# Kernel optimization log

Hardware: AMD Instinct MI355X
Metric: run time of the kernel (lower is better)

## Reference

```python
import jax, jax.numpy as jnp
import numpy as np

N = 50000
E = 800000
IN_DIM = 128
HID = 256
NCLASS = 40
ORDER = 3
LOCAL_NOISE = 0.5


def setup_inputs() -> dict:
    key = jax.random.key(0)
    ks = jax.random.split(key, 8)
    feats = jax.random.normal(ks[0], (N, IN_DIM), dtype=jnp.float32)
    edge_row = jax.random.randint(ks[1], (E,), 0, N, dtype=jnp.int32)
    edge_col = jax.random.randint(ks[2], (E,), 0, N, dtype=jnp.int32)
    edge_vals = jax.random.uniform(ks[3], (E,), dtype=jnp.float32) / 16.0  # ~row-normalized adjacency
    W1 = jax.random.normal(ks[4], (IN_DIM, HID), dtype=jnp.float32) * (1.0 / np.sqrt(IN_DIM))
    b1 = jnp.zeros((HID,), dtype=jnp.float32)
    W2 = jax.random.normal(ks[5], (HID, NCLASS), dtype=jnp.float32) * (1.0 / np.sqrt(HID))
    b2 = jnp.zeros((NCLASS,), dtype=jnp.float32)
    return {"feats": feats, "edge_row": edge_row, "edge_col": edge_col,
            "edge_vals": edge_vals, "W1": W1, "b1": b1, "W2": W2, "b2": b2}


def _spmm(edge_row, edge_col, edge_vals, x):
    # y[r] = sum_e vals[e] * x[col[e]] for edges with row[e]==r
    msgs = edge_vals[:, None] * x[edge_col]  # [E, D]
    return jax.ops.segment_sum(msgs, edge_row, num_segments=N)


def reference(feats, edge_row, edge_col, edge_vals, W1, b1, W2, b2):
    # eval path: drop_node scales by (1 - drop_rate)
    x = feats * (1.0 - LOCAL_NOISE)
    # GRANDConv_NX: K-hop propagation with running-sum average
    y = x
    h = x
    for _ in range(ORDER):
        h = _spmm(edge_row, edge_col, edge_vals, h)
        y = y + h
    feat = y / (ORDER + 1.0)
    # MLP (use_bn=False, dropout inactive at eval)
    h1 = jax.nn.relu(feat @ W1 + b1)
    logits = h1 @ W2 + b2
    # MLP.forward applies log_softmax, outer forward applies it again
    out = jax.nn.log_softmax(jax.nn.log_softmax(logits, axis=-1), axis=-1)
    return out
```

## Files before the change

kernel.cpp:

```cpp
#include <hip/hip_runtime.h>
#include <math.h>

#define N_NODES 50000
#define N_EDGES 800000
#define IN_DIM 128
#define HID 256
#define NCLASS 40

#define SCAN_NBLK 49

#define HBLK 256
#define EPB  3125
#define PK   12500

typedef __attribute__((ext_vector_type(8))) short short8;
typedef __attribute__((ext_vector_type(4))) float floatx4;

__device__ inline unsigned bf16pair(float a, float b) {
    unsigned ua = __float_as_uint(a), ub = __float_as_uint(b);
    ua = (ua + 0x7fffu + ((ua >> 16) & 1u)) >> 16;
    ub = (ub + 0x7fffu + ((ub >> 16) & 1u)) >> 16;
    return ua | (ub << 16);
}
__device__ inline unsigned bf16bits(float a) {
    unsigned ua = __float_as_uint(a);
    return (ua + 0x7fffu + ((ua >> 16) & 1u)) >> 16;
}
__device__ inline float bf_lo(unsigned u) { return __uint_as_float(u << 16); }
__device__ inline float bf_hi(unsigned u) { return __uint_as_float(u & 0xffff0000u); }

__global__ void prep_kernel(const float4* __restrict__ f4,
                            uint2* __restrict__ fb16,
                            const float* __restrict__ W1,
                            uint4* __restrict__ W1frag) {
    int i = blockIdx.x * blockDim.x + threadIdx.x;
    float4 v = f4[i];
    fb16[i] = make_uint2(bf16pair(v.x, v.y), bf16pair(v.z, v.w));
    if (i < 4096) {
        int f = i;
        int h = f >> 11, rem = f & 2047;
        int t = rem >> 8, s = (rem >> 6) & 3, l = rem & 63;
        int q = l >> 4, n16 = l & 15;
        int n = h * 128 + t * 16 + n16;
        int kb = s * 32 + q * 8;
        unsigned p[4];
        #pragma unroll
        for (int jj = 0; jj < 4; ++jj) {
            float a = W1[(size_t)(kb + 2 * jj) * HID + n];
            float b = W1[(size_t)(kb + 2 * jj + 1) * HID + n];
            p[jj] = bf16pair(a, b);
        }
        W1frag[f] = make_uint4(p[0], p[1], p[2], p[3]);
    }
}

__global__ __launch_bounds__(1024) void hist_kernel(const int* __restrict__ rows,
                                                    unsigned* __restrict__ hist) {
    __shared__ unsigned h[PK];
    int t = threadIdx.x;
    for (int i = t; i < PK / 4; i += 1024)
        ((uint4*)h)[i] = make_uint4(0u, 0u, 0u, 0u);
    __syncthreads();
    int e0 = blockIdx.x * EPB;
    for (int i = t; i < EPB; i += 1024) {
        int r = rows[e0 + i];
        atomicAdd(&h[r >> 2], 1u << ((r & 3) * 8));
    }
    __syncthreads();
    unsigned* out = hist + (size_t)blockIdx.x * PK;
    for (int i = t; i < PK / 4; i += 1024)
        ((uint4*)out)[i] = ((const uint4*)h)[i];
}

__global__ void colscan_kernel(const unsigned* __restrict__ hist,
                               unsigned* __restrict__ base,
                               int* __restrict__ counts,
                               int* __restrict__ blockSums) {
    int t = blockIdx.x * 256 + threadIdx.x;
    unsigned run = 0;
    if (t < PK) {
        #pragma unroll 8
        for (int b = 0; b < HBLK; ++b) {
            unsigned v = hist[b * PK + t];
            base[b * PK + t] = run;
            run += v;
        }
        *(int4*)(counts + 4 * t) = make_int4((int)(run & 0xffu), (int)((run >> 8) & 0xffu),
                                             (int)((run >> 16) & 0xffu), (int)(run >> 24));
    }
    int s = (int)((run & 0xffu) + ((run >> 8) & 0xffu) + ((run >> 16) & 0xffu) + (run >> 24));
    #pragma unroll
    for (int off = 32; off >= 1; off >>= 1)
        s += __shfl_xor(s, off);
    __shared__ int wsum[4];
    int lane = threadIdx.x & 63, wid = threadIdx.x >> 6;
    if (lane == 0) wsum[wid] = s;
    __syncthreads();
    if (threadIdx.x == 0)
        blockSums[blockIdx.x] = wsum[0] + wsum[1] + wsum[2] + wsum[3];
}

__global__ void block_offset_kernel(const int* __restrict__ blockSums,
                                    int* __restrict__ blockOffs,
                                    int* __restrict__ row_start) {
    int lane = threadIdx.x;
    int x = (lane < SCAN_NBLK) ? blockSums[lane] : 0;
    #pragma unroll
    for (int off = 1; off < 64; off <<= 1) {
        int y = __shfl_up(x, off);
        if (lane >= off) x += y;
    }
    int excl = __shfl_up(x, 1);
    if (lane == 0) excl = 0;
    if (lane < SCAN_NBLK) blockOffs[lane] = excl;
    if (lane == SCAN_NBLK - 1) row_start[N_NODES] = x;
}

__global__ void local_scan_kernel(const int* __restrict__ counts,
                                  const int* __restrict__ blockOffs,
                                  int* __restrict__ row_start) {
    int t = threadIdx.x;
    int base = blockIdx.x * 1024 + t * 4;
    int4 c = make_int4(0, 0, 0, 0);
    if (base < N_NODES) c = *(const int4*)(counts + base);
    int s0 = c.x, s1 = s0 + c.y, s2 = s1 + c.z, s3 = s2 + c.w;
    int tsum = s3;
    int lane = t & 63, wid = t >> 6;
    int x = tsum;
    #pragma unroll
    for (int off = 1; off < 64; off <<= 1) {
        int y = __shfl_up(x, off);
        if (lane >= off) x += y;
    }
    __shared__ int wsum[4];
    if (lane == 63) wsum[wid] = x;
    __syncthreads();
    int woff = 0;
    for (int i = 0; i < 4; ++i)
        if (i < wid) woff += wsum[i];
    int excl = x - tsum + woff + blockOffs[blockIdx.x];
    if (base < N_NODES) {
        int4 rs = make_int4(excl, excl + s0, excl + s1, excl + s2);
        *(int4*)(row_start + base) = rs;
    }
}

__global__ __launch_bounds__(1024) void scatter2_kernel(const int* __restrict__ rows,
                                                        const int* __restrict__ cols,
                                                        const float* __restrict__ vals,
                                                        const unsigned* __restrict__ base,
                                                        const int* __restrict__ row_start,
                                                        unsigned* __restrict__ csr_cv) {
    __shared__ unsigned cur[PK];
    int t = threadIdx.x;
    const uint4* bb = (const uint4*)(base + (size_t)blockIdx.x * PK);
    for (int i = t; i < PK / 4; i += 1024)
        ((uint4*)cur)[i] = bb[i];
    __syncthreads();
    int e0 = blockIdx.x * EPB;
    for (int i = t; i < EPB; i += 1024) {
        int e = e0 + i;
        int r = rows[e];
        unsigned sh = (unsigned)(r & 3) * 8u;
        unsigned old = atomicAdd(&cur[r >> 2], 1u << sh);
        int pos = row_start[r] + (int)((old >> sh) & 0xffu);
        csr_cv[pos] = ((unsigned)cols[e] << 16) | bf16bits(vals[e]);
    }
}

template <int MODE>
__global__ void spmm_csr(const int* __restrict__ row_start,
                         const unsigned* __restrict__ csr_cv,
                         const uint4* __restrict__ Hin4,
                         uint4* __restrict__ Hout4,
                         const float* __restrict__ feats,
                         const uint4* __restrict__ h1b4,
                         const uint4* __restrict__ h2b4) {
    int wave = (blockIdx.x * blockDim.x + threadIdx.x) >> 6;
    int lane = threadIdx.x & 63;
    if (wave >= N_NODES) return;
    int p = lane >> 4;
    int q = lane & 15;
    int start = row_start[wave];
    int end   = row_start[wave + 1];
    float acc[8] = {};
    for (int base = start; base < end; base += 64) {
        int idx = base + lane;
        unsigned u = 0;
        if (idx < end) u = csr_cv[idx];
        int cnt = min(64, end - base);
        for (int j = 0; j < cnt; j += 8) {
            unsigned uj0 = __shfl(u, j + p);
            unsigned uj1 = __shfl(u, j + 4 + p);
            int   c0 = uj0 >> 16;
            int   c1 = uj1 >> 16;
            float v0 = __uint_as_float(uj0 << 16);
            float v1 = __uint_as_float(uj1 << 16);
            uint4 h0 = Hin4[(size_t)c0 * 16 + q];
            uint4 h1 = Hin4[(size_t)c1 * 16 + q];
            acc[0] += v0 * bf_lo(h0.x);
            acc[1] += v0 * bf_hi(h0.x);
            acc[2] += v0 * bf_lo(h0.y);
            acc[3] += v0 * bf_hi(h0.y);
            acc[4] += v0 * bf_lo(h0.z);
            acc[5] += v0 * bf_hi(h0.z);
            acc[6] += v0 * bf_lo(h0.w);
            acc[7] += v0 * bf_hi(h0.w);
            acc[0] += v1 * bf_lo(h1.x);
            acc[1] += v1 * bf_hi(h1.x);
            acc[2] += v1 * bf_lo(h1.y);
            acc[3] += v1 * bf_hi(h1.y);
            acc[4] += v1 * bf_lo(h1.z);
            acc[5] += v1 * bf_hi(h1.z);
            acc[6] += v1 * bf_lo(h1.w);
            acc[7] += v1 * bf_hi(h1.w);
        }
    }
    #pragma unroll
    for (int i = 0; i < 8; ++i) {
        acc[i] += __shfl_xor(acc[i], 16);
        acc[i] += __shfl_xor(acc[i], 32);
    }
    if (p == 0) {
        size_t o16 = (size_t)wave * 16 + q;
        if (MODE == 1) {
            #pragma unroll
            for (int i = 0; i < 8; ++i) acc[i] *= 0.5f;
        } else if (MODE == 2) {
            size_t of = (size_t)wave * IN_DIM + q * 8;
            float4 f0 = *(const float4*)(feats + of);
            float4 f1 = *(const float4*)(feats + of + 4);
            uint4 a = h1b4[o16];
            uint4 b = h2b4[o16];
            acc[0] += 0.5f * f0.x + bf_lo(a.x) + bf_lo(b.x);
            acc[1] += 0.5f * f0.y + bf_hi(a.x) + bf_hi(b.x);
            acc[2] += 0.5f * f0.z + bf_lo(a.y) + bf_lo(b.y);
            acc[3] += 0.5f * f0.w + bf_hi(a.y) + bf_hi(b.y);
            acc[4] += 0.5f * f1.x + bf_lo(a.z) + bf_lo(b.z);
            acc[5] += 0.5f * f1.y + bf_hi(a.z) + bf_hi(b.z);
            acc[6] += 0.5f * f1.z + bf_lo(a.w) + bf_lo(b.w);
            acc[7] += 0.5f * f1.w + bf_hi(a.w) + bf_hi(b.w);
        }
        Hout4[o16] = make_uint4(bf16pair(acc[0], acc[1]), bf16pair(acc[2], acc[3]),
                                bf16pair(acc[4], acc[5]), bf16pair(acc[6], acc[7]));
    }
}

__global__ void gemm1_mfma(const uint4* __restrict__ yb4,
                           const uint4* __restrict__ W1frag,
                           const float* __restrict__ bias1,
                           float* __restrict__ H1) {
    __shared__ uint4 wlds[2048];
    int tid = threadIdx.x;
    int h = blockIdx.y;
    for (int i = tid; i < 2048; i += 256)
        wlds[i] = W1frag[h * 2048 + i];
    __syncthreads();

    int wave = tid >> 6, lane = tid & 63;
    int q = lane >> 4, c16 = lane & 15;
    int row0 = blockIdx.x * 64 + wave * 16;
    int arow = row0 + c16;

    union { uint4 u; short8 v; } au[4], bu;
    if (arow < N_NODES) {
        #pragma unroll
        for (int s = 0; s < 4; ++s)
            au[s].u = yb4[(size_t)arow * 16 + 4 * s + q];
    } else {
        #pragma unroll
        for (int s = 0; s < 4; ++s)
            au[s].u = make_uint4(0u, 0u, 0u, 0u);
    }

    #pragma unroll
    for (int t = 0; t < 8; ++t) {
        floatx4 acc = {0.f, 0.f, 0.f, 0.f};
        #pragma unroll
        for (int s = 0; s < 4; ++s) {
            bu.u = wlds[(t * 4 + s) * 64 + lane];
            acc = __builtin_amdgcn_mfma_f32_16x16x32_bf16(au[s].v, bu.v, acc, 0, 0, 0);
        }
        int col = h * 128 + t * 16 + c16;
        float bs = bias1[col];
        #pragma unroll
        for (int r = 0; r < 4; ++r) {
            int crow = row0 + q * 4 + r;
            if (crow < N_NODES) {
                float v = 0.25f * acc[r] + bs;
                H1[(size_t)crow * HID + col] = v > 0.f ? v : 0.f;
            }
        }
    }
}

#define G2_BM 128
#define G2_BK 32
__global__ void gemm2_kernel(const float* __restrict__ H1,
                             const float* __restrict__ W2,
                             float* __restrict__ part0,
                             float* __restrict__ part1) {
    __shared__ float As[G2_BK][G2_BM + 4];
    __shared__ float Bs[G2_BK][44];
    int tid = threadIdx.x;
    int rt = tid >> 3;
    int ct = tid & 7;
    int row0 = blockIdx.x * G2_BM;
    int kbase = blockIdx.y * (HID / 2);
    float* outp = blockIdx.y ? part1 : part0;
    float acc[4][5] = {};
    for (int kt = 0; kt < HID / 2; kt += G2_BK) {
        int k0 = kbase + kt;
        #pragma unroll
        for (int i = tid; i < 1024; i += 256) {
            int r = i >> 3, u = i & 7;
            int gr = row0 + r;
            float4 v = make_float4(0.f, 0.f, 0.f, 0.f);
            if (gr < N_NODES)
                v = *(const float4*)(H1 + (size_t)gr * HID + k0 + u * 4);
            int kb = u * 4;
            As[kb + 0][r] = v.x;
            As[kb + 1][r] = v.y;
            As[kb + 2][r] = v.z;
            As[kb + 3][r] = v.w;
        }
        for (int i = tid; i < 320; i += 256) {
            int r = i / 10, cg = i % 10;
            float4 w = *(const float4*)(W2 + (size_t)(k0 + r) * NCLASS + cg * 4);
            *(float4*)&Bs[r][cg * 4] = w;
        }
        __syncthreads();
        #pragma unroll
        for (int kk = 0; kk < G2_BK; ++kk) {
            float4 a0 = *(const float4*)&As[kk][rt * 4];
            float a[4] = {a0.x, a0.y, a0.z, a0.w};
            float b[5];
            #pragma unroll
            for (int j = 0; j < 5; ++j) b[j] = Bs[kk][ct * 5 + j];
            #pragma unroll
            for (int i = 0; i < 4; ++i)
                #pragma unroll
                for (int j = 0; j < 5; ++j)
                    acc[i][j] += a[i] * b[j];
        }
        __syncthreads();
    }
    #pragma unroll
    for (int i = 0; i < 4; ++i) {
        int gr = row0 + rt * 4 + i;
        if (gr >= N_NODES) continue;
        float* dst = outp + (size_t)gr * NCLASS + ct * 5;
        #pragma unroll
        for (int j = 0; j < 5; ++j)
            dst[j] = acc[i][j];
    }
}

__global__ void lsm_kernel(const float* __restrict__ part0,
                           const float* __restrict__ part1,
                           const float* __restrict__ b2,
                           float* __restrict__ Out) {
    int wave = threadIdx.x >> 6;
    int lane = threadIdx.x & 63;
    int row = blockIdx.x * 4 + wave;
    if (row >= N_NODES) return;

    float acc = -INFINITY;
    if (lane < NCLASS) {
        size_t idx = (size_t)row * NCLASS + lane;
        acc = part0[idx] + part1[idx] + b2[lane];
    }

    float m = acc;
    #pragma unroll
    for (int off = 32; off >= 1; off >>= 1)
        m = fmaxf(m, __shfl_xor(m, off));
    float ex = (lane < NCLASS) ? expf(acc - m) : 0.f;
    float s = ex;
    #pragma unroll
    for (int off = 32; off >= 1; off >>= 1)
        s += __shfl_xor(s, off);
    float z1 = acc - (m + logf(s));

    float m2 = z1;
    #pragma unroll
    for (int off = 32; off >= 1; off >>= 1)
        m2 = fmaxf(m2, __shfl_xor(m2, off));
    float ex2 = (lane < NCLASS) ? expf(z1 - m2) : 0.f;
    float s2 = ex2;
    #pragma unroll
    for (int off = 32; off >= 1; off >>= 1)
        s2 += __shfl_xor(s2, off);
    float z2 = z1 - (m2 + logf(s2));

    if (lane < NCLASS)
        Out[(size_t)row * NCLASS + lane] = z2;
}

extern "C" void kernel_launch(void* const* d_in, const int* in_sizes, int n_in,
                              void* d_out, int out_size, void* d_ws, size_t ws_size,
                              hipStream_t stream) {
    const float* feats   = (const float*)d_in[0];
    const int*   e_row   = (const int*)d_in[1];
    const int*   e_col   = (const int*)d_in[2];
    const float* e_vals  = (const float*)d_in[3];
    const float* W1      = (const float*)d_in[4];
    const float* b1      = (const float*)d_in[5];
    const float* W2      = (const float*)d_in[6];
    const float* b2      = (const float*)d_in[7];
    float* out = (float*)d_out;

    float* ws    = (float*)d_ws;
    uint4* ybf4  = (uint4*)ws;
    unsigned* hist = (unsigned*)ws;
    uint4* W1frag = (uint4*)(ws + (size_t)N_NODES * IN_DIM / 2);
    int*   counts = (int*)(ws + 3300000);
    uint4* fb16_4 = (uint4*)(ws + (size_t)N_NODES * IN_DIM);
    uint4* h1b4  = (uint4*)(ws + (size_t)N_NODES * IN_DIM * 3 / 2);
    uint4* h2b4  = (uint4*)(ws + (size_t)N_NODES * IN_DIM * 2);
    unsigned* basep = (unsigned*)(ws + (size_t)N_NODES * IN_DIM * 5 / 2);
    float* hid   = ws + (size_t)N_NODES * IN_DIM;
    float* part0 = ws;
    float* part1 = ws + (size_t)N_NODES * NCLASS;

    unsigned* csr_cv = (unsigned*)d_out;
    int*   row_start = (int*)d_out + 2 * N_EDGES;
    int*   blockSums = row_start + N_NODES + 4;
    int*   blockOffs = blockSums + 64;

    const int ELEMS4 = N_NODES * IN_DIM / 4;
    prep_kernel<<<ELEMS4 / 256, 256, 0, stream>>>((const float4*)feats, (uint2*)fb16_4,
                                                  W1, W1frag);

    hist_kernel<<<HBLK, 1024, 0, stream>>>(e_row, hist);
    colscan_kernel<<<SCAN_NBLK, 256, 0, stream>>>(hist, basep, counts, blockSums);
    block_offset_kernel<<<1, 64, 0, stream>>>(blockSums, blockOffs, row_start);
    local_scan_kernel<<<SCAN_NBLK, 256, 0, stream>>>(counts, blockOffs, row_start);
    scatter2_kernel<<<HBLK, 1024, 0, stream>>>(e_row, e_col, e_vals, basep,
                                               row_start, csr_cv);

    const int SPMM_BLOCKS = N_NODES / 4;
    spmm_csr<1><<<SPMM_BLOCKS, 256, 0, stream>>>(row_start, csr_cv, fb16_4, h1b4,
                                                 nullptr, nullptr, nullptr);
    spmm_csr<0><<<SPMM_BLOCKS, 256, 0, stream>>>(row_start, csr_cv, h1b4, h2b4,
                                                 nullptr, nullptr, nullptr);
    spmm_csr<2><<<SPMM_BLOCKS, 256, 0, stream>>>(row_start, csr_cv, h2b4, ybf4,
                                                 feats, h1b4, h2b4);

    dim3 g1((N_NODES + 63) / 64, 2);
    gemm1_mfma<<<g1, 256, 0, stream>>>(ybf4, W1frag, b1, hid);

    dim3 g2((N_NODES + G2_BM - 1) / G2_BM, 2);
    gemm2_kernel<<<g2, 256, 0, stream>>>(hid, W2, part0, part1);

    lsm_kernel<<<(N_NODES + 3) / 4, 256, 0, stream>>>(part0, part1, b2, out);
}
```

Baseline: 278.0 us.

## Fuse gemm2 with log-softmax, merge scan kernels, widen SpMM unroll with nontemporal access

The column scan now splits the 256 histogram blocks across four groups per block, adding a group-offset buffer that the scatter kernel applies. The block-offset scan is folded into the local scan kernel. The SpMM inner loop now handles four edges per step and uses nontemporal loads and stores. The split-K gemm2 and the separate double log-softmax kernel are merged into one kernel that reduces across 8 lanes, removing the partial-sum buffers and two launches at the cost of lower gemm2 parallelism.

```diff
diff --git a/kernel.cpp b/kernel.cpp
--- a/kernel.cpp
+++ b/kernel.cpp
@@ -12,9 +12,12 @@
 #define HBLK 256
 #define EPB  3125
 #define PK   12500
+#define CS_G 4
+#define CS_HPG 64
 
 typedef __attribute__((ext_vector_type(8))) short short8;
 typedef __attribute__((ext_vector_type(4))) float floatx4;
+typedef __attribute__((ext_vector_type(4))) unsigned uintx4;
 
 __device__ inline unsigned bf16pair(float a, float b) {
     unsigned ua = __float_as_uint(a), ub = __float_as_uint(b);
@@ -72,54 +75,78 @@
         ((uint4*)out)[i] = ((const uint4*)h)[i];
 }
 
-__global__ void colscan_kernel(const unsigned* __restrict__ hist,
-                               unsigned* __restrict__ base,
-                               int* __restrict__ counts,
-                               int* __restrict__ blockSums) {
-    int t = blockIdx.x * 256 + threadIdx.x;
+__global__ __launch_bounds__(1024) void colscan_kernel(const unsigned* __restrict__ hist,
+                                                       unsigned* __restrict__ base,
+                                                       unsigned* __restrict__ goff,
+                                                       int* __restrict__ counts,
+                                                       int* __restrict__ blockSums) {
+    __shared__ unsigned lsum[CS_G][256];
+    int tid = threadIdx.x;
+    int g = tid >> 8;
+    int c = tid & 255;
+    int colq = blockIdx.x * 256 + c;
     unsigned run = 0;
-    if (t < PK) {
+    if (colq < PK) {
         #pragma unroll 8
-        for (int b = 0; b < HBLK; ++b) {
-            unsigned v = hist[b * PK + t];
-            base[b * PK + t] = run;
+        for (int i = 0; i < CS_HPG; ++i) {
+            int b = g * CS_HPG + i;
+            unsigned v = hist[(size_t)b * PK + colq];
+            base[(size_t)b * PK + colq] = run;
             run += v;
         }
-        *(int4*)(counts + 4 * t) = make_int4((int)(run & 0xffu), (int)((run >> 8) & 0xffu),
-                                             (int)((run >> 16) & 0xffu), (int)(run >> 24));
-    }
-    int s = (int)((run & 0xffu) + ((run >> 8) & 0xffu) + ((run >> 16) & 0xffu) + (run >> 24));
-    #pragma unroll
-    for (int off = 32; off >= 1; off >>= 1)
-        s += __shfl_xor(s, off);
+    }
+    lsum[g][c] = run;
+    __syncthreads();
+    unsigned off = 0;
+    #pragma unroll
+    for (int gg = 0; gg < CS_G; ++gg) {
+        unsigned v = lsum[gg][c];
+        if (gg < g) off += v;
+    }
+    unsigned tot = off + run;
+    if (colq < PK) {
+        goff[(size_t)g * PK + colq] = off;
+        if (g == CS_G - 1)
+            *(int4*)(counts + 4 * colq) = make_int4((int)(tot & 0xffu), (int)((tot >> 8) & 0xffu),
+                                                    (int)((tot >> 16) & 0xffu), (int)(tot >> 24));
+    }
+    int s = 0;
+    if (g == CS_G - 1 && colq < PK)
+        s = (int)((tot & 0xffu) + ((tot >> 8) & 0xffu) + ((tot >> 16) & 0xffu) + (tot >> 24));
+    #pragma unroll
+    for (int o = 32; o >= 1; o >>= 1)
+        s += __shfl_xor(s, o);
+    __shared__ int wsum[16];
+    int lane = tid & 63, wid = tid >> 6;
+    if (lane == 0) wsum[wid] = s;
+    __syncthreads();
+    if (tid == 0) {
+        int acc = 0;
+        #pragma unroll
+        for (int i = 0; i < 16; ++i) acc += wsum[i];
+        blockSums[blockIdx.x] = acc;
+    }
+}
+
+__global__ __launch_bounds__(256) void local_scan_kernel(const int* __restrict__ counts,
+                                                         const int* __restrict__ blockSums,
+                                                         int* __restrict__ row_start) {
     __shared__ int wsum[4];
-    int lane = threadIdx.x & 63, wid = threadIdx.x >> 6;
-    if (lane == 0) wsum[wid] = s;
-    __syncthreads();
-    if (threadIdx.x == 0)
-        blockSums[blockIdx.x] = wsum[0] + wsum[1] + wsum[2] + wsum[3];
-}
-
-__global__ void block_offset_kernel(const int* __restrict__ blockSums,
-                                    int* __restrict__ blockOffs,
-                                    int* __restrict__ row_start) {
-    int lane = threadIdx.x;
-    int x = (lane < SCAN_NBLK) ? blockSums[lane] : 0;
-    #pragma unroll
-    for (int off = 1; off < 64; off <<= 1) {
-        int y = __shfl_up(x, off);
-        if (lane >= off) x += y;
-    }
-    int excl = __shfl_up(x, 1);
-    if (lane == 0) excl = 0;
-    if (lane < SCAN_NBLK) blockOffs[lane] = excl;
-    if (lane == SCAN_NBLK - 1) row_start[N_NODES] = x;
-}
-
-__global__ void local_scan_kernel(const int* __restrict__ counts,
-                                  const int* __restrict__ blockOffs,
-                                  int* __restrict__ row_start) {
+    __shared__ int boff;
     int t = threadIdx.x;
+    if (t < 64) {
+        int x = (t < SCAN_NBLK) ? blockSums[t] : 0;
+        #pragma unroll
+        for (int off = 1; off < 64; off <<= 1) {
+            int y = __shfl_up(x, off);
+            if (t >= off) x += y;
+        }
+        int excl = __shfl_up(x, 1);
+        if (t == 0) excl = 0;
+        if (t == blockIdx.x) boff = excl;
+        if (blockIdx.x == SCAN_NBLK - 1 && t == SCAN_NBLK - 1)
+            row_start[N_NODES] = x;
+    }
     int base = blockIdx.x * 1024 + t * 4;
     int4 c = make_int4(0, 0, 0, 0);
     if (base < N_NODES) c = *(const int4*)(counts + base);
@@ -132,13 +159,12 @@
         int y = __shfl_up(x, off);
         if (lane >= off) x += y;
     }
-    __shared__ int wsum[4];
     if (lane == 63) wsum[wid] = x;
     __syncthreads();
     int woff = 0;
     for (int i = 0; i < 4; ++i)
         if (i < wid) woff += wsum[i];
-    int excl = x - tsum + woff + blockOffs[blockIdx.x];
+    int excl = x - tsum + woff + boff;
     if (base < N_NODES) {
         int4 rs = make_int4(excl, excl + s0, excl + s1, excl + s2);
         *(int4*)(row_start + base) = rs;
@@ -149,13 +175,17 @@
                                                         const int* __restrict__ cols,
                                                         const float* __restrict__ vals,
                                                         const unsigned* __restrict__ base,
+                                                        const unsigned* __restrict__ goff,
                                                         const int* __restrict__ row_start,
                                                         unsigned* __restrict__ csr_cv) {
     __shared__ unsigned cur[PK];
     int t = threadIdx.x;
     const uint4* bb = (const uint4*)(base + (size_t)blockIdx.x * PK);
-    for (int i = t; i < PK / 4; i += 1024)
-        ((uint4*)cur)[i] = bb[i];
+    const uint4* gg = (const uint4*)(goff + (size_t)(blockIdx.x >> 6) * PK);
+    for (int i = t; i < PK / 4; i += 1024) {
+        uint4 b = bb[i], o = gg[i];
+        ((uint4*)cur)[i] = make_uint4(b.x + o.x, b.y + o.y, b.z + o.z, b.w + o.w);
+    }
     __syncthreads();
     int e0 = blockIdx.x * EPB;
     for (int i = t; i < EPB; i += 1024) {
@@ -171,11 +201,11 @@
 template <int MODE>
 __global__ void spmm_csr(const int* __restrict__ row_start,
                          const unsigned* __restrict__ csr_cv,
-                         const uint4* __restrict__ Hin4,
-                         uint4* __restrict__ Hout4,
+                         const uintx4* __restrict__ Hin4,
+                         uintx4* __restrict__ Hout4,
                          const float* __restrict__ feats,
-                         const uint4* __restrict__ h1b4,
-                         const uint4* __restrict__ h2b4) {
+                         const uintx4* __restrict__ h1b4,
+                         const uintx4* __restrict__ h2b4) {
     int wave = (blockIdx.x * blockDim.x + threadIdx.x) >> 6;
     int lane = threadIdx.x & 63;
     if (wave >= N_NODES) return;
@@ -187,33 +217,38 @@
     for (int base = start; base < end; base += 64) {
         int idx = base + lane;
         unsigned u = 0;
-        if (idx < end) u = csr_cv[idx];
+        if (idx < end) u = __builtin_nontemporal_load(csr_cv + idx);
         int cnt = min(64, end - base);
-        for (int j = 0; j < cnt; j += 8) {
+        for (int j = 0; j < cnt; j += 16) {
             unsigned uj0 = __shfl(u, j + p);
             unsigned uj1 = __shfl(u, j + 4 + p);
-            int   c0 = uj0 >> 16;
-            int   c1 = uj1 >> 16;
+            unsigned uj2 = __shfl(u, j + 8 + p);
+            unsigned uj3 = __shfl(u, j + 12 + p);
+            int c0 = uj0 >> 16, c1 = uj1 >> 16, c2 = uj2 >> 16, c3 = uj3 >> 16;
             float v0 = __uint_as_float(uj0 << 16);
             float v1 = __uint_as_float(uj1 << 16);
-            uint4 h0 = Hin4[(size_t)c0 * 16 + q];
-            uint4 h1 = Hin4[(size_t)c1 * 16 + q];
-            acc[0] += v0 * bf_lo(h0.x);
-            acc[1] += v0 * bf_hi(h0.x);
-            acc[2] += v0 * bf_lo(h0.y);
-            acc[3] += v0 * bf_hi(h0.y);
-            acc[4] += v0 * bf_lo(h0.z);
-            acc[5] += v0 * bf_hi(h0.z);
-            acc[6] += v0 * bf_lo(h0.w);
-            acc[7] += v0 * bf_hi(h0.w);
-            acc[0] += v1 * bf_lo(h1.x);
-            acc[1] += v1 * bf_hi(h1.x);
-            acc[2] += v1 * bf_lo(h1.y);
-            acc[3] += v1 * bf_hi(h1.y);
-            acc[4] += v1 * bf_lo(h1.z);
-            acc[5] += v1 * bf_hi(h1.z);
-            acc[6] += v1 * bf_lo(h1.w);
-            acc[7] += v1 * bf_hi(h1.w);
+            float v2 = __uint_as_float(uj2 << 16);
+            float v3 = __uint_as_float(uj3 << 16);
+            uintx4 h0 = Hin4[(size_t)c0 * 16 + q];
+            uintx4 h1 = Hin4[(size_t)c1 * 16 + q];
+            uintx4 h2 = Hin4[(size_t)c2 * 16 + q];
+            uintx4 h3 = Hin4[(size_t)c3 * 16 + q];
+            acc[0] += v0 * bf_lo(h0.x); acc[1] += v0 * bf_hi(h0.x);
+            acc[2] += v0 * bf_lo(h0.y); acc[3] += v0 * bf_hi(h0.y);
+            acc[4] += v0 * bf_lo(h0.z); acc[5] += v0 * bf_hi(h0.z);
+            acc[6] += v0 * bf_lo(h0.w); acc[7] += v0 * bf_hi(h0.w);
+            acc[0] += v1 * bf_lo(h1.x); acc[1] += v1 * bf_hi(h1.x);
+            acc[2] += v1 * bf_lo(h1.y); acc[3] += v1 * bf_hi(h1.y);
+            acc[4] += v1 * bf_lo(h1.z); acc[5] += v1 * bf_hi(h1.z);
+            acc[6] += v1 * bf_lo(h1.w); acc[7] += v1 * bf_hi(h1.w);
+            acc[0] += v2 * bf_lo(h2.x); acc[1] += v2 * bf_hi(h2.x);
+            acc[2] += v2 * bf_lo(h2.y); acc[3] += v2 * bf_hi(h2.y);
+            acc[4] += v2 * bf_lo(h2.z); acc[5] += v2 * bf_hi(h2.z);
+            acc[6] += v2 * bf_lo(h2.w); acc[7] += v2 * bf_hi(h2.w);
+            acc[0] += v3 * bf_lo(h3.x); acc[1] += v3 * bf_hi(h3.x);
+            acc[2] += v3 * bf_lo(h3.y); acc[3] += v3 * bf_hi(h3.y);
+            acc[4] += v3 * bf_lo(h3.z); acc[5] += v3 * bf_hi(h3.z);
+            acc[6] += v3 * bf_lo(h3.w); acc[7] += v3 * bf_hi(h3.w);
         }
     }
     #pragma unroll
@@ -228,10 +263,10 @@
             for (int i = 0; i < 8; ++i) acc[i] *= 0.5f;
         } else if (MODE == 2) {
             size_t of = (size_t)wave * IN_DIM + q * 8;
-            float4 f0 = *(const float4*)(feats + of);
-            float4 f1 = *(const float4*)(feats + of + 4);
-            uint4 a = h1b4[o16];
-            uint4 b = h2b4[o16];
+            floatx4 f0 = __builtin_nontemporal_load((const floatx4*)(feats + of));
+            floatx4 f1 = __builtin_nontemporal_load((const floatx4*)(feats + of + 4));
+            uintx4 a = __builtin_nontemporal_load(h1b4 + o16);
+            uintx4 b = __builtin_nontemporal_load(h2b4 + o16);
             acc[0] += 0.5f * f0.x + bf_lo(a.x) + bf_lo(b.x);
             acc[1] += 0.5f * f0.y + bf_hi(a.x) + bf_hi(b.x);
             acc[2] += 0.5f * f0.z + bf_lo(a.y) + bf_lo(b.y);
@@ -241,8 +276,12 @@
             acc[6] += 0.5f * f1.z + bf_lo(a.w) + bf_lo(b.w);
             acc[7] += 0.5f * f1.w + bf_hi(a.w) + bf_hi(b.w);
         }
-        Hout4[o16] = make_uint4(bf16pair(acc[0], acc[1]), bf16pair(acc[2], acc[3]),
-                                bf16pair(acc[4], acc[5]), bf16pair(acc[6], acc[7]));
+        uintx4 rv;
+        rv.x = bf16pair(acc[0], acc[1]);
+        rv.y = bf16pair(acc[2], acc[3]);
+        rv.z = bf16pair(acc[4], acc[5]);
+        rv.w = bf16pair(acc[6], acc[7]);
+        __builtin_nontemporal_store(rv, Hout4 + o16);
     }
 }
 
@@ -295,22 +334,18 @@
 }
 
 #define G2_BM 128
-#define G2_BK 32
-__global__ void gemm2_kernel(const float* __restrict__ H1,
-                             const float* __restrict__ W2,
-                             float* __restrict__ part0,
-                             float* __restrict__ part1) {
-    __shared__ float As[G2_BK][G2_BM + 4];
-    __shared__ float Bs[G2_BK][44];
+__global__ void gemm2lsm_kernel(const float* __restrict__ H1,
+                                const float* __restrict__ W2,
+                                const float* __restrict__ b2,
+                                float* __restrict__ Out) {
+    __shared__ float As[32][G2_BM + 4];
+    __shared__ float Bs[32][44];
     int tid = threadIdx.x;
     int rt = tid >> 3;
     int ct = tid & 7;
     int row0 = blockIdx.x * G2_BM;
-    int kbase = blockIdx.y * (HID / 2);
-    float* outp = blockIdx.y ? part1 : part0;
     float acc[4][5] = {};
-    for (int kt = 0; kt < HID / 2; kt += G2_BK) {
-        int k0 = kbase + kt;
+    for (int k0 = 0; k0 < HID; k0 += 32) {
         #pragma unroll
         for (int i = tid; i < 1024; i += 256) {
             int r = i >> 3, u = i & 7;
@@ -331,7 +366,7 @@
         }
         __syncthreads();
         #pragma unroll
-        for (int kk = 0; kk < G2_BK; ++kk) {
+        for (int kk = 0; kk < 32; ++kk) {
             float4 a0 = *(const float4*)&As[kk][rt * 4];
             float a[4] = {a0.x, a0.y, a0.z, a0.w};
             float b[5];
@@ -345,56 +380,45 @@
         }
         __syncthreads();
     }
+    float bb[5];
+    #pragma unroll
+    for (int j = 0; j < 5; ++j) bb[j] = b2[ct * 5 + j];
     #pragma unroll
     for (int i = 0; i < 4; ++i) {
         int gr = row0 + rt * 4 + i;
-        if (gr >= N_NODES) continue;
-        float* dst = outp + (size_t)gr * NCLASS + ct * 5;
-        #pragma unroll
-        for (int j = 0; j < 5; ++j)
-            dst[j] = acc[i][j];
-    }
-}
-
-__global__ void lsm_kernel(const float* __restrict__ part0,
-                           const float* __restrict__ part1,
-                           const float* __restrict__ b2,
-                           float* __restrict__ Out) {
-    int wave = threadIdx.x >> 6;
-    int lane = threadIdx.x & 63;
-    int row = blockIdx.x * 4 + wave;
-    if (row >= N_NODES) return;
-
-    float acc = -INFINITY;
-    if (lane < NCLASS) {
-        size_t idx = (size_t)row * NCLASS + lane;
-        acc = part0[idx] + part1[idx] + b2[lane];
-    }
-
-    float m = acc;
-    #pragma unroll
-    for (int off = 32; off >= 1; off >>= 1)
-        m = fmaxf(m, __shfl_xor(m, off));
-    float ex = (lane < NCLASS) ? expf(acc - m) : 0.f;
-    float s = ex;
-    #pragma unroll
-    for (int off = 32; off >= 1; off >>= 1)
-        s += __shfl_xor(s, off);
-    float z1 = acc - (m + logf(s));
-
-    float m2 = z1;
-    #pragma unroll
-    for (int off = 32; off >= 1; off >>= 1)
-        m2 = fmaxf(m2, __shfl_xor(m2, off));
-    float ex2 = (lane < NCLASS) ? expf(z1 - m2) : 0.f;
-    float s2 = ex2;
-    #pragma unroll
-    for (int off = 32; off >= 1; off >>= 1)
-        s2 += __shfl_xor(s2, off);
-    float z2 = z1 - (m2 + logf(s2));
-
-    if (lane < NCLASS)
-        Out[(size_t)row * NCLASS + lane] = z2;
+        float z[5];
+        #pragma unroll
+        for (int j = 0; j < 5; ++j) z[j] = acc[i][j] + bb[j];
+        float m = z[0];
+        #pragma unroll
+        for (int j = 1; j < 5; ++j) m = fmaxf(m, z[j]);
+        #pragma unroll
+        for (int off = 1; off < 8; off <<= 1) m = fmaxf(m, __shfl_xor(m, off));
+        float s = 0.f;
+        #pragma unroll
+        for (int j = 0; j < 5; ++j) s += expf(z[j] - m);
+        #pragma unroll
+        for (int off = 1; off < 8; off <<= 1) s += __shfl_xor(s, off);
+        float l1 = m + logf(s);
+        #pragma unroll
+        for (int j = 0; j < 5; ++j) z[j] -= l1;
+        float m2 = z[0];
+        #pragma unroll
+        for (int j = 1; j < 5; ++j) m2 = fmaxf(m2, z[j]);
+        #pragma unroll
+        for (int off = 1; off < 8; off <<= 1) m2 = fmaxf(m2, __shfl_xor(m2, off));
+        float s2 = 0.f;
+        #pragma unroll
+        for (int j = 0; j < 5; ++j) s2 += expf(z[j] - m2);
+        #pragma unroll
+        for (int off = 1; off < 8; off <<= 1) s2 += __shfl_xor(s2, off);
+        float l2 = m2 + logf(s2);
+        if (gr < N_NODES) {
+            float* dst = Out + (size_t)gr * NCLASS + ct * 5;
+            #pragma unroll
+            for (int j = 0; j < 5; ++j) dst[j] = z[j] - l2;
+        }
+    }
 }
 
 extern "C" void kernel_launch(void* const* d_in, const int* in_sizes, int n_in,
@@ -415,43 +439,38 @@
     unsigned* hist = (unsigned*)ws;
     uint4* W1frag = (uint4*)(ws + (size_t)N_NODES * IN_DIM / 2);
     int*   counts = (int*)(ws + 3300000);
+    unsigned* goff = (unsigned*)(ws + 3400000);
     uint4* fb16_4 = (uint4*)(ws + (size_t)N_NODES * IN_DIM);
     uint4* h1b4  = (uint4*)(ws + (size_t)N_NODES * IN_DIM * 3 / 2);
     uint4* h2b4  = (uint4*)(ws + (size_t)N_NODES * IN_DIM * 2);
     unsigned* basep = (unsigned*)(ws + (size_t)N_NODES * IN_DIM * 5 / 2);
     float* hid   = ws + (size_t)N_NODES * IN_DIM;
-    float* part0 = ws;
-    float* part1 = ws + (size_t)N_NODES * NCLASS;
 
     unsigned* csr_cv = (unsigned*)d_out;
     int*   row_start = (int*)d_out + 2 * N_EDGES;
     int*   blockSums = row_start + N_NODES + 4;
-    int*   blockOffs = blockSums + 64;
 
     const int ELEMS4 = N_NODES * IN_DIM / 4;
     prep_kernel<<<ELEMS4 / 256, 256, 0, stream>>>((const float4*)feats, (uint2*)fb16_4,
                                                   W1, W1frag);
 
     hist_kernel<<<HBLK, 1024, 0, stream>>>(e_row, hist);
-    colscan_kernel<<<SCAN_NBLK, 256, 0, stream>>>(hist, basep, counts, blockSums);
-    block_offset_kernel<<<1, 64, 0, stream>>>(blockSums, blockOffs, row_start);
-    local_scan_kernel<<<SCAN_NBLK, 256, 0, stream>>>(counts, blockOffs, row_start);
-    scatter2_kernel<<<HBLK, 1024, 0, stream>>>(e_row, e_col, e_vals, basep,
+    colscan_kernel<<<SCAN_NBLK, 1024, 0, stream>>>(hist, basep, goff, counts, blockSums);
+    local_scan_kernel<<<SCAN_NBLK, 256, 0, stream>>>(counts, blockSums, row_start);
+    scatter2_kernel<<<HBLK, 1024, 0, stream>>>(e_row, e_col, e_vals, basep, goff,
                                                row_start, csr_cv);
 
     const int SPMM_BLOCKS = N_NODES / 4;
-    spmm_csr<1><<<SPMM_BLOCKS, 256, 0, stream>>>(row_start, csr_cv, fb16_4, h1b4,
-                                                 nullptr, nullptr, nullptr);
-    spmm_csr<0><<<SPMM_BLOCKS, 256, 0, stream>>>(row_start, csr_cv, h1b4, h2b4,
-                                                 nullptr, nullptr, nullptr);
-    spmm_csr<2><<<SPMM_BLOCKS, 256, 0, stream>>>(row_start, csr_cv, h2b4, ybf4,
-                                                 feats, h1b4, h2b4);
+    spmm_csr<1><<<SPMM_BLOCKS, 256, 0, stream>>>(row_start, csr_cv, (const uintx4*)fb16_4,
+                                                 (uintx4*)h1b4, nullptr, nullptr, nullptr);
+    spmm_csr<0><<<SPMM_BLOCKS, 256, 0, stream>>>(row_start, csr_cv, (const uintx4*)h1b4,
+                                                 (uintx4*)h2b4, nullptr, nullptr, nullptr);
+    spmm_csr<2><<<SPMM_BLOCKS, 256, 0, stream>>>(row_start, csr_cv, (const uintx4*)h2b4,
+                                                 (uintx4*)ybf4, feats,
+                                                 (const uintx4*)h1b4, (const uintx4*)h2b4);
 
     dim3 g1((N_NODES + 63) / 64, 2);
     gemm1_mfma<<<g1, 256, 0, stream>>>(ybf4, W1frag, b1, hid);
 
-    dim3 g2((N_NODES + G2_BM - 1) / G2_BM, 2);
-    gemm2_kernel<<<g2, 256, 0, stream>>>(hid, W2, part0, part1);
-
-    lsm_kernel<<<(N_NODES + 3) / 4, 256, 0, stream>>>(part0, part1, b2, out);
-}
+    gemm2lsm_kernel<<<(N_NODES + G2_BM - 1) / G2_BM, 256, 0, stream>>>(hid, W2, b2, out);
+}
```

Result: faster. 268.9 us (-3.3%).
